# Performance work log

Hardware: AMD Instinct MI355X
Metric: run time of the kernel (lower is better)

Reference implementation:

```python
import jax, jax.numpy as jnp
import numpy as np

EMBED_DIM = 1024
HEAD_DIM = 64


def setup_inputs() -> dict:
    key = jax.random.key(0)
    k1, k2, k3, k4 = jax.random.split(key, 4)
    hidden_state = jax.random.normal(k1, (4, 4096, EMBED_DIM), dtype=jnp.float32)
    s = 1.0 / np.sqrt(EMBED_DIM)
    Wq = jax.random.uniform(k2, (EMBED_DIM, HEAD_DIM), dtype=jnp.float32, minval=-s, maxval=s)
    Wk = jax.random.uniform(k3, (EMBED_DIM, HEAD_DIM), dtype=jnp.float32, minval=-s, maxval=s)
    Wv = jax.random.uniform(k4, (EMBED_DIM, HEAD_DIM), dtype=jnp.float32, minval=-s, maxval=s)
    return {"hidden_state": hidden_state, "Wq": Wq, "Wk": Wk, "Wv": Wv}


def reference(hidden_state, Wq, Wk, Wv):
    # hidden_state: [B, S, E]; Wq/Wk/Wv: [E, D]
    q = hidden_state @ Wq  # [B, S, D]
    k = hidden_state @ Wk
    v = hidden_state @ Wv
    seq_len = hidden_state.shape[-2]
    scale = 1.0 / jnp.sqrt(jnp.asarray(HEAD_DIM, dtype=q.dtype))
    scores = jnp.einsum("bqd,bkd->bqk", q, k) * scale  # [B, S, S]
    causal = jnp.tril(jnp.ones((seq_len, seq_len), dtype=bool))  # [S, S]
    scores = jnp.where(causal[None, :, :], scores, jnp.asarray(-jnp.inf, dtype=scores.dtype))
    weights = jax.nn.softmax(scores, axis=-1)
    return jnp.einsum("bqk,bkd->bqd", weights, v)  # [B, S, D]
```

## Files before the change

kernel.cpp:

```cpp
#include <hip/hip_runtime.h>
#include <hip/hip_bf16.h>
#include <stdint.h>

#define SEQ 4096
#define EMB 1024
#define HD  64
#define NB  4

typedef __attribute__((ext_vector_type(8))) short short8;
typedef __attribute__((ext_vector_type(4))) float f32x4;
typedef __attribute__((ext_vector_type(4))) unsigned int uint4v;

static __device__ __forceinline__ unsigned short f2bf(float f) {
    unsigned int u = __float_as_uint(f);
    u += 0x7fffu + ((u >> 16) & 1u);
    return (unsigned short)(u >> 16);
}

__global__ __launch_bounds__(256) void wprep_kernel(
        const float* __restrict__ Wq, const float* __restrict__ Wk,
        const float* __restrict__ Wv, unsigned short* __restrict__ Wt) {
    int idx = blockIdx.x * 256 + threadIdx.x;
    int m = idx >> 16;
    int r = idx & 65535;
    int d = r >> 10;
    int e = r & 1023;
    const float* W = (m == 0) ? Wq : (m == 1) ? Wk : Wv;
    float v = W[e * HD + d];
    if (m == 0) v *= 0.18033688011111793f;
    Wt[idx] = f2bf(v);
}

__global__ __launch_bounds__(512, 4) void qkv_kernel(
        const float* __restrict__ H, const unsigned short* __restrict__ Wt,
        unsigned short* __restrict__ Qb, unsigned short* __restrict__ Kb,
        unsigned short* __restrict__ Vt) {
    __shared__ unsigned char smem[122880];
    unsigned short* ldsW = (unsigned short*)smem;
    float* ldsH = (float*)(smem + 3 * 24576);
    float* ldsO = (float*)smem;

    const int tid  = threadIdx.x;
    const int w    = tid >> 6;
    const int lane = tid & 63;
    const int lr = lane & 15, lg = lane >> 4;
    const int rt = w >> 1, ch = w & 1;
    const int rowbase = blockIdx.x * 64;

    f32x4 acc[6];
    #pragma unroll
    for (int nt = 0; nt < 6; ++nt) acc[nt] = f32x4{0.f, 0.f, 0.f, 0.f};

    auto stage = [&](int buf, int c) {
        const int kk0 = c * 64;
        #pragma unroll
        for (int ii = 0; ii < 3; ++ii) {
            int i = w * 3 + ii;
            int rowidx = 8 * i + (lane >> 3);
            int sb = (lane & 7) ^ (lane >> 3);
            const unsigned short* src = Wt + rowidx * EMB + kk0 + sb * 8;
            __builtin_amdgcn_global_load_lds(
                (const __attribute__((address_space(1))) void*)src,
                (__attribute__((address_space(3))) void*)(ldsW + buf * 12288 + i * 512 + lane * 8),
                16, 0, 0);
        }
        #pragma unroll
        for (int ii = 0; ii < 2; ++ii) {
            int i = w * 2 + ii;
            int rowidx = 4 * i + (lane >> 4);
            int key = rowidx & 7;
            int sb = (lane & 15) ^ key;
            const float* src = H + (size_t)(rowbase + rowidx) * EMB + kk0 + sb * 4;
            __builtin_amdgcn_global_load_lds(
                (const __attribute__((address_space(1))) void*)src,
                (__attribute__((address_space(3))) void*)(ldsH + buf * 4096 + i * 256 + lane * 4),
                16, 0, 0);
        }
    };

    auto compute = [&](int buf) {
        const int hrow = rt * 16 + lr;
        const int hkey = lr & 7;
        #pragma unroll
        for (int ks = 0; ks < 2; ++ks) {
            int b0 = ks * 8 + lg * 2;
            f32x4 h0 = *(const f32x4*)(ldsH + buf * 4096 + hrow * 64 + ((b0 ^ hkey) * 4));
            f32x4 h1 = *(const f32x4*)(ldsH + buf * 4096 + hrow * 64 + (((b0 + 1) ^ hkey) * 4));
            uint4v ua;
            asm("v_cvt_pk_bf16_f32 %0, %1, %2" : "=v"(ua[0]) : "v"(h0[0]), "v"(h0[1]));
            asm("v_cvt_pk_bf16_f32 %0, %1, %2" : "=v"(ua[1]) : "v"(h0[2]), "v"(h0[3]));
            asm("v_cvt_pk_bf16_f32 %0, %1, %2" : "=v"(ua[2]) : "v"(h1[0]), "v"(h1[1]));
            asm("v_cvt_pk_bf16_f32 %0, %1, %2" : "=v"(ua[3]) : "v"(h1[2]), "v"(h1[3]));
            short8 af = *(short8*)&ua;
            #pragma unroll
            for (int nt = 0; nt < 6; ++nt) {
                int f = ch * 6 + nt;
                int row = f * 16 + lr;
                int blk = (ks * 4 + lg) ^ hkey;
                short8 bf_ = *(const short8*)(ldsW + buf * 12288 + row * 64 + blk * 8);
                acc[nt] = __builtin_amdgcn_mfma_f32_16x16x32_bf16(af, bf_, acc[nt], 0, 0, 0);
            }
        }
    };

    stage(0, 0);
    stage(1, 1);
    for (int c = 0; c < 16; ++c) {
        if (c + 2 < 16) stage((c + 2) % 3, c + 2);
        if (c <= 13)      asm volatile("s_waitcnt vmcnt(10)" ::: "memory");
        else if (c == 14) asm volatile("s_waitcnt vmcnt(5)"  ::: "memory");
        else              asm volatile("s_waitcnt vmcnt(0)"  ::: "memory");
        __builtin_amdgcn_sched_barrier(0);
        __builtin_amdgcn_s_barrier();
        compute(c % 3);
        __builtin_amdgcn_s_barrier();
    }

    #pragma unroll
    for (int nt = 0; nt < 6; ++nt)
        #pragma unroll
        for (int r = 0; r < 4; ++r)
            ldsO[(rt * 16 + lg * 4 + r) * 200 + ch * 96 + nt * 16 + lr] = acc[nt][r];
    __syncthreads();

    {
        const int row = tid >> 3;
        const int d0  = (tid & 7) * 8;
        const size_t grow = (size_t)(rowbase + row);
        short8 uq, uk;
        #pragma unroll
        for (int j = 0; j < 8; ++j) {
            uq[j] = (short)f2bf(ldsO[row * 200 + d0 + j]);
            uk[j] = (short)f2bf(ldsO[row * 200 + 64 + d0 + j]);
        }
        *(short8*)(Qb + grow * HD + d0) = uq;
        *(short8*)(Kb + grow * HD + (d0 ^ ((row & 7) << 3))) = uk;
    }
    {
        const int d  = tid >> 3;
        const int j  = tid & 7;
        const int b  = rowbase >> 12;
        const int ci = (rowbase & (SEQ - 1)) >> 6;
        unsigned short* vrow = Vt + (((size_t)b * 64 + ci) * 64 + d) * 64;
        const int dsw = (d & 7) << 3;
        #pragma unroll
        for (int k4 = 0; k4 < 4; ++k4) {
            int t0 = j * 2 + k4 * 16;
            int tt = t0 & 31;
            int p0 = ((tt & 12) << 1) | (tt & 3) | ((tt & 16) >> 2);
            int e  = ((t0 & 32) | p0) ^ dsw;
            unsigned int val = (unsigned int)f2bf(ldsO[t0 * 200 + 128 + d])
                             | ((unsigned int)f2bf(ldsO[(t0 + 1) * 200 + 128 + d]) << 16);
            *(unsigned int*)(vrow + e) = val;
        }
    }
}

__global__ __launch_bounds__(512, 2) void attn_kernel(
        const unsigned short* __restrict__ Qb, const unsigned short* __restrict__ Kb,
        const unsigned short* __restrict__ Vt,
        float* __restrict__ part_o, float* __restrict__ part_l) {
    __shared__ unsigned short ldsK[3 * 64 * 64];
    __shared__ unsigned short ldsV[3 * 64 * 64];
    const int tid  = threadIdx.x;
    const int w    = tid >> 6;
    const int lane = tid & 63;
    const int lr = lane & 15, lg = lane >> 4;

    const int bid   = blockIdx.x;
    const int b     = bid & 3;
    const int qbr   = (bid >> 2) & 31;
    const int slice = bid >> 7;
    const int qb    = (slice >= 2) ? (31 - qbr) : qbr;
    const int qrow0 = qb * 128 + w * 16;
    const int qwmax = qrow0 + 15;

    const unsigned short* __restrict__ Kp = Kb + (size_t)b * SEQ * HD;
    const unsigned short* __restrict__ Vp = Vt + (size_t)b * 64 * 4096;
    const unsigned short* __restrict__ Qp = Qb + ((size_t)b * SEQ + qrow0) * HD;

    short8 qf0 = *(const short8*)(Qp + lr * HD +      lg * 8);
    short8 qf1 = *(const short8*)(Qp + lr * HD + 32 + lg * 8);

    f32x4 o[4];
    #pragma unroll
    for (int nt = 0; nt < 4; ++nt) o[nt] = f32x4{0.f, 0.f, 0.f, 0.f};
    float lrun = 0.f;

    const int T  = 2 * (qb + 1);
    const int sz = (T + 3) >> 2;
    const int c0 = slice * sz;
    const int c1 = (c0 + sz < T) ? (c0 + sz) : T;
    const int nch = c1 - c0;
    const int swz = (lr & 7) << 3;

    auto stage = [&](int buf, int it) {
        const unsigned short* gk = Kp + (size_t)it * 64 * HD + w * 512 + lane * 8;
        const unsigned short* gv = Vp + (size_t)it * 4096 + w * 512 + lane * 8;
        __builtin_amdgcn_global_load_lds(
            (const __attribute__((address_space(1))) void*)gk,
            (__attribute__((address_space(3))) void*)(ldsK + buf * 4096 + w * 512), 16, 0, 0);
        __builtin_amdgcn_global_load_lds(
            (const __attribute__((address_space(1))) void*)gv,
            (__attribute__((address_space(3))) void*)(ldsV + buf * 4096 + w * 512), 16, 0, 0);
    };

    if (nch > 0) {
        stage(0, c0);
        if (nch > 1) stage(1, c0 + 1);
        for (int i = 0; i < nch; ++i) {
            if (i + 2 < nch) stage((i + 2) % 3, c0 + i + 2);
            if (i + 2 < nch)      asm volatile("s_waitcnt vmcnt(4)" ::: "memory");
            else if (i + 1 < nch) asm volatile("s_waitcnt vmcnt(2)" ::: "memory");
            else                  asm volatile("s_waitcnt vmcnt(0)" ::: "memory");
            __builtin_amdgcn_sched_barrier(0);
            __builtin_amdgcn_s_barrier();

            const int kvb = (c0 + i) * 64;
            const int bufo = (i % 3) * 4096;
            if (kvb <= qwmax) {
                f32x4 s0 = f32x4{0.f, 0.f, 0.f, 0.f};
                f32x4 s1 = f32x4{0.f, 0.f, 0.f, 0.f};
                f32x4 s2 = f32x4{0.f, 0.f, 0.f, 0.f};
                f32x4 s3 = f32x4{0.f, 0.f, 0.f, 0.f};
                {
                    short8 ka0 = *(const short8*)&ldsK[bufo + (0 * 16 + lr) * 64 + ((lg * 8)      ^ swz)];
                    short8 kb0 = *(const short8*)&ldsK[bufo + (0 * 16 + lr) * 64 + ((lg * 8 + 32) ^ swz)];
                    short8 ka1 = *(const short8*)&ldsK[bufo + (1 * 16 + lr) * 64 + ((lg * 8)      ^ swz)];
                    short8 kb1 = *(const short8*)&ldsK[bufo + (1 * 16 + lr) * 64 + ((lg * 8 + 32) ^ swz)];
                    short8 ka2 = *(const short8*)&ldsK[bufo + (2 * 16 + lr) * 64 + ((lg * 8)      ^ swz)];
                    short8 kb2 = *(const short8*)&ldsK[bufo + (2 * 16 + lr) * 64 + ((lg * 8 + 32) ^ swz)];
                    short8 ka3 = *(const short8*)&ldsK[bufo + (3 * 16 + lr) * 64 + ((lg * 8)      ^ swz)];
                    short8 kb3 = *(const short8*)&ldsK[bufo + (3 * 16 + lr) * 64 + ((lg * 8 + 32) ^ swz)];
                    s0 = __builtin_amdgcn_mfma_f32_16x16x32_bf16(ka0, qf0, s0, 0, 0, 0);
                    s0 = __builtin_amdgcn_mfma_f32_16x16x32_bf16(kb0, qf1, s0, 0, 0, 0);
                    s1 = __builtin_amdgcn_mfma_f32_16x16x32_bf16(ka1, qf0, s1, 0, 0, 0);
                    s1 = __builtin_amdgcn_mfma_f32_16x16x32_bf16(kb1, qf1, s1, 0, 0, 0);
                    s2 = __builtin_amdgcn_mfma_f32_16x16x32_bf16(ka2, qf0, s2, 0, 0, 0);
                    s2 = __builtin_amdgcn_mfma_f32_16x16x32_bf16(kb2, qf1, s2, 0, 0, 0);
                    s3 = __builtin_amdgcn_mfma_f32_16x16x32_bf16(ka3, qf0, s3, 0, 0, 0);
                    s3 = __builtin_amdgcn_mfma_f32_16x16x32_bf16(kb3, qf1, s3, 0, 0, 0);
                }

                if (kvb + 63 > qrow0) {
                    const int qg = qrow0 + lr;
                    #pragma unroll
                    for (int r = 0; r < 4; ++r) {
                        int ky = kvb + lg * 4 + r;
                        if (ky      > qg) s0[r] = -1e30f;
                        if (ky + 16 > qg) s1[r] = -1e30f;
                        if (ky + 32 > qg) s2[r] = -1e30f;
                        if (ky + 48 > qg) s3[r] = -1e30f;
                    }
                }

                float p0[4], p1[4], p2[4], p3[4];
                #pragma unroll
                for (int r = 0; r < 4; ++r) {
                    p0[r] = exp2f(s0[r]);
                    p1[r] = exp2f(s1[r]);
                    p2[r] = exp2f(s2[r]);
                    p3[r] = exp2f(s3[r]);
                }
                lrun += ((p0[0] + p0[1]) + (p0[2] + p0[3])) + ((p1[0] + p1[1]) + (p1[2] + p1[3]))
                      + ((p2[0] + p2[1]) + (p2[2] + p2[3])) + ((p3[0] + p3[1]) + (p3[2] + p3[3]));

                uint4v ua, ub;
                asm("v_cvt_pk_bf16_f32 %0, %1, %2" : "=v"(ua[0]) : "v"(p0[0]), "v"(p0[1]));
                asm("v_cvt_pk_bf16_f32 %0, %1, %2" : "=v"(ua[1]) : "v"(p0[2]), "v"(p0[3]));
                asm("v_cvt_pk_bf16_f32 %0, %1, %2" : "=v"(ua[2]) : "v"(p1[0]), "v"(p1[1]));
                asm("v_cvt_pk_bf16_f32 %0, %1, %2" : "=v"(ua[3]) : "v"(p1[2]), "v"(p1[3]));
                asm("v_cvt_pk_bf16_f32 %0, %1, %2" : "=v"(ub[0]) : "v"(p2[0]), "v"(p2[1]));
                asm("v_cvt_pk_bf16_f32 %0, %1, %2" : "=v"(ub[1]) : "v"(p2[2]), "v"(p2[3]));
                asm("v_cvt_pk_bf16_f32 %0, %1, %2" : "=v"(ub[2]) : "v"(p3[0]), "v"(p3[1]));
                asm("v_cvt_pk_bf16_f32 %0, %1, %2" : "=v"(ub[3]) : "v"(p3[2]), "v"(p3[3]));
                short8 pba = *(short8*)&ua;
                short8 pbb = *(short8*)&ub;

                short8 va0 = *(const short8*)&ldsV[bufo + (0 * 16 + lr) * 64 + ((lg * 8)      ^ swz)];
                short8 vb0 = *(const short8*)&ldsV[bufo + (0 * 16 + lr) * 64 + ((lg * 8 + 32) ^ swz)];
                short8 va1 = *(const short8*)&ldsV[bufo + (1 * 16 + lr) * 64 + ((lg * 8)      ^ swz)];
                short8 vb1 = *(const short8*)&ldsV[bufo + (1 * 16 + lr) * 64 + ((lg * 8 + 32) ^ swz)];
                short8 va2 = *(const short8*)&ldsV[bufo + (2 * 16 + lr) * 64 + ((lg * 8)      ^ swz)];
                short8 vb2 = *(const short8*)&ldsV[bufo + (2 * 16 + lr) * 64 + ((lg * 8 + 32) ^ swz)];
                short8 va3 = *(const short8*)&ldsV[bufo + (3 * 16 + lr) * 64 + ((lg * 8)      ^ swz)];
                short8 vb3 = *(const short8*)&ldsV[bufo + (3 * 16 + lr) * 64 + ((lg * 8 + 32) ^ swz)];
                o[0] = __builtin_amdgcn_mfma_f32_16x16x32_bf16(va0, pba, o[0], 0, 0, 0);
                o[1] = __builtin_amdgcn_mfma_f32_16x16x32_bf16(va1, pba, o[1], 0, 0, 0);
                o[2] = __builtin_amdgcn_mfma_f32_16x16x32_bf16(va2, pba, o[2], 0, 0, 0);
                o[3] = __builtin_amdgcn_mfma_f32_16x16x32_bf16(va3, pba, o[3], 0, 0, 0);
                o[0] = __builtin_amdgcn_mfma_f32_16x16x32_bf16(vb0, pbb, o[0], 0, 0, 0);
                o[1] = __builtin_amdgcn_mfma_f32_16x16x32_bf16(vb1, pbb, o[1], 0, 0, 0);
                o[2] = __builtin_amdgcn_mfma_f32_16x16x32_bf16(vb2, pbb, o[2], 0, 0, 0);
                o[3] = __builtin_amdgcn_mfma_f32_16x16x32_bf16(vb3, pbb, o[3], 0, 0, 0);
            }
            __builtin_amdgcn_s_barrier();
        }
    }

    lrun += __shfl_xor(lrun, 16);
    lrun += __shfl_xor(lrun, 32);

    const size_t prow = (((size_t)slice * 4 + b) * 32 + qb) * 128 + w * 16 + lr;
    float* po = part_o + prow * 64;
    #pragma unroll
    for (int nt = 0; nt < 4; ++nt)
        *(f32x4*)(po + nt * 16 + lg * 4) = o[nt];
    if (lg == 0) part_l[prow] = lrun;
}

__global__ __launch_bounds__(256) void merge_kernel(
        const float* __restrict__ part_o, const float* __restrict__ part_l,
        float* __restrict__ out) {
    int idx = blockIdx.x * 256 + threadIdx.x;
    int d4  = (idx & 15) * 4;
    int row = idx >> 4;
    f32x4 a = f32x4{0.f, 0.f, 0.f, 0.f};
    float L = 0.f;
    #pragma unroll
    for (int s = 0; s < 4; ++s) {
        f32x4 p = *(const f32x4*)(part_o + ((size_t)s * 16384 + row) * 64 + d4);
        a[0] += p[0]; a[1] += p[1]; a[2] += p[2]; a[3] += p[3];
        L += part_l[s * 16384 + row];
    }
    float inv = 1.0f / L;
    f32x4 r;
    r[0] = a[0] * inv;
    r[1] = a[1] * inv;
    r[2] = a[2] * inv;
    r[3] = a[3] * inv;
    *(f32x4*)(out + (size_t)row * 64 + d4) = r;
}

extern "C" void kernel_launch(void* const* d_in, const int* in_sizes, int n_in,
                              void* d_out, int out_size, void* d_ws, size_t ws_size,
                              hipStream_t stream) {
    const float* H  = (const float*)d_in[0];
    const float* Wq = (const float*)d_in[1];
    const float* Wk = (const float*)d_in[2];
    const float* Wv = (const float*)d_in[3];
    float* out = (float*)d_out;

    unsigned short* Qb = (unsigned short*)d_ws;
    unsigned short* Kb = Qb + (size_t)NB * SEQ * HD;
    unsigned short* Vt = Kb + (size_t)NB * SEQ * HD;
    unsigned short* Wt = Vt + (size_t)NB * SEQ * HD;
    float* part_o = (float*)(Wt + 3 * 65536);
    float* part_l = part_o + (size_t)4 * 16384 * 64;

    wprep_kernel<<<768, 256, 0, stream>>>(Wq, Wk, Wv, Wt);
    qkv_kernel<<<NB * SEQ / 64, 512, 0, stream>>>(H, Wt, Qb, Kb, Vt);
    attn_kernel<<<512, 512, 0, stream>>>(Qb, Kb, Vt, part_o, part_l);
    merge_kernel<<<1024, 256, 0, stream>>>(part_o, part_l, out);
}
```

Baseline: 52.65 us.

## Stage KV tiles in pairs with double buffering to halve barriers

Restructures the attention loop so each iteration loads and processes two 64-row K/V tiles. A two-slot double buffer replaces the three-slot single-tile ring, which halves the number of workgroup barriers and waitcnt points per chunk. LDS per block grows from 48KB to 64KB, which may reduce occupancy at two blocks per CU. The prefetch distance in tiles stays similar, but each wait now covers a larger batch.

```diff
diff --git a/kernel.cpp b/kernel.cpp
--- a/kernel.cpp
+++ b/kernel.cpp
@@ -160,8 +160,8 @@
         const unsigned short* __restrict__ Qb, const unsigned short* __restrict__ Kb,
         const unsigned short* __restrict__ Vt,
         float* __restrict__ part_o, float* __restrict__ part_l) {
-    __shared__ unsigned short ldsK[3 * 64 * 64];
-    __shared__ unsigned short ldsV[3 * 64 * 64];
+    __shared__ unsigned short ldsK[2 * 2 * 4096];
+    __shared__ unsigned short ldsV[2 * 2 * 4096];
     const int tid  = threadIdx.x;
     const int w    = tid >> 6;
     const int lane = tid & 63;
@@ -192,107 +192,123 @@
     const int c0 = slice * sz;
     const int c1 = (c0 + sz < T) ? (c0 + sz) : T;
     const int nch = c1 - c0;
+    const int nin = (nch + 1) >> 1;
+    const bool tail_odd = (nch & 1) != 0;
     const int swz = (lr & 7) << 3;
 
-    auto stage = [&](int buf, int it) {
-        const unsigned short* gk = Kp + (size_t)it * 64 * HD + w * 512 + lane * 8;
-        const unsigned short* gv = Vp + (size_t)it * 4096 + w * 512 + lane * 8;
-        __builtin_amdgcn_global_load_lds(
-            (const __attribute__((address_space(1))) void*)gk,
-            (__attribute__((address_space(3))) void*)(ldsK + buf * 4096 + w * 512), 16, 0, 0);
-        __builtin_amdgcn_global_load_lds(
-            (const __attribute__((address_space(1))) void*)gv,
-            (__attribute__((address_space(3))) void*)(ldsV + buf * 4096 + w * 512), 16, 0, 0);
+    auto stage_pair = [&](int buf, int j) {
+        #pragma unroll
+        for (int jj = 0; jj < 2; ++jj) {
+            int ci = c0 + 2 * j + jj;
+            if (ci < c1) {
+                const unsigned short* gk = Kp + (size_t)ci * 64 * HD + w * 512 + lane * 8;
+                const unsigned short* gv = Vp + (size_t)ci * 4096 + w * 512 + lane * 8;
+                __builtin_amdgcn_global_load_lds(
+                    (const __attribute__((address_space(1))) void*)gk,
+                    (__attribute__((address_space(3))) void*)(ldsK + buf * 8192 + jj * 4096 + w * 512), 16, 0, 0);
+                __builtin_amdgcn_global_load_lds(
+                    (const __attribute__((address_space(1))) void*)gv,
+                    (__attribute__((address_space(3))) void*)(ldsV + buf * 8192 + jj * 4096 + w * 512), 16, 0, 0);
+            }
+        }
     };
 
     if (nch > 0) {
-        stage(0, c0);
-        if (nch > 1) stage(1, c0 + 1);
-        for (int i = 0; i < nch; ++i) {
-            if (i + 2 < nch) stage((i + 2) % 3, c0 + i + 2);
-            if (i + 2 < nch)      asm volatile("s_waitcnt vmcnt(4)" ::: "memory");
-            else if (i + 1 < nch) asm volatile("s_waitcnt vmcnt(2)" ::: "memory");
-            else                  asm volatile("s_waitcnt vmcnt(0)" ::: "memory");
+        stage_pair(0, 0);
+        for (int j = 0; j < nin; ++j) {
+            if (j + 1 < nin) stage_pair((j + 1) & 1, j + 1);
+            if (j + 1 < nin) {
+                if (tail_odd && (j + 2 == nin)) asm volatile("s_waitcnt vmcnt(2)" ::: "memory");
+                else                            asm volatile("s_waitcnt vmcnt(4)" ::: "memory");
+            } else {
+                asm volatile("s_waitcnt vmcnt(0)" ::: "memory");
+            }
             __builtin_amdgcn_sched_barrier(0);
             __builtin_amdgcn_s_barrier();
 
-            const int kvb = (c0 + i) * 64;
-            const int bufo = (i % 3) * 4096;
-            if (kvb <= qwmax) {
-                f32x4 s0 = f32x4{0.f, 0.f, 0.f, 0.f};
-                f32x4 s1 = f32x4{0.f, 0.f, 0.f, 0.f};
-                f32x4 s2 = f32x4{0.f, 0.f, 0.f, 0.f};
-                f32x4 s3 = f32x4{0.f, 0.f, 0.f, 0.f};
-                {
-                    short8 ka0 = *(const short8*)&ldsK[bufo + (0 * 16 + lr) * 64 + ((lg * 8)      ^ swz)];
-                    short8 kb0 = *(const short8*)&ldsK[bufo + (0 * 16 + lr) * 64 + ((lg * 8 + 32) ^ swz)];
-                    short8 ka1 = *(const short8*)&ldsK[bufo + (1 * 16 + lr) * 64 + ((lg * 8)      ^ swz)];
-                    short8 kb1 = *(const short8*)&ldsK[bufo + (1 * 16 + lr) * 64 + ((lg * 8 + 32) ^ swz)];
-                    short8 ka2 = *(const short8*)&ldsK[bufo + (2 * 16 + lr) * 64 + ((lg * 8)      ^ swz)];
-                    short8 kb2 = *(const short8*)&ldsK[bufo + (2 * 16 + lr) * 64 + ((lg * 8 + 32) ^ swz)];
-                    short8 ka3 = *(const short8*)&ldsK[bufo + (3 * 16 + lr) * 64 + ((lg * 8)      ^ swz)];
-                    short8 kb3 = *(const short8*)&ldsK[bufo + (3 * 16 + lr) * 64 + ((lg * 8 + 32) ^ swz)];
-                    s0 = __builtin_amdgcn_mfma_f32_16x16x32_bf16(ka0, qf0, s0, 0, 0, 0);
-                    s0 = __builtin_amdgcn_mfma_f32_16x16x32_bf16(kb0, qf1, s0, 0, 0, 0);
-                    s1 = __builtin_amdgcn_mfma_f32_16x16x32_bf16(ka1, qf0, s1, 0, 0, 0);
-                    s1 = __builtin_amdgcn_mfma_f32_16x16x32_bf16(kb1, qf1, s1, 0, 0, 0);
-                    s2 = __builtin_amdgcn_mfma_f32_16x16x32_bf16(ka2, qf0, s2, 0, 0, 0);
-                    s2 = __builtin_amdgcn_mfma_f32_16x16x32_bf16(kb2, qf1, s2, 0, 0, 0);
-                    s3 = __builtin_amdgcn_mfma_f32_16x16x32_bf16(ka3, qf0, s3, 0, 0, 0);
-                    s3 = __builtin_amdgcn_mfma_f32_16x16x32_bf16(kb3, qf1, s3, 0, 0, 0);
-                }
-
-                if (kvb + 63 > qrow0) {
-                    const int qg = qrow0 + lr;
-                    #pragma unroll
-                    for (int r = 0; r < 4; ++r) {
-                        int ky = kvb + lg * 4 + r;
-                        if (ky      > qg) s0[r] = -1e30f;
-                        if (ky + 16 > qg) s1[r] = -1e30f;
-                        if (ky + 32 > qg) s2[r] = -1e30f;
-                        if (ky + 48 > qg) s3[r] = -1e30f;
+            #pragma unroll
+            for (int jj = 0; jj < 2; ++jj) {
+                const int ci = c0 + 2 * j + jj;
+                if (ci < c1) {
+                    const int kvb = ci * 64;
+                    const int bufo = ((j & 1) * 2 + jj) * 4096;
+                    if (kvb <= qwmax) {
+                        f32x4 s0 = f32x4{0.f, 0.f, 0.f, 0.f};
+                        f32x4 s1 = f32x4{0.f, 0.f, 0.f, 0.f};
+                        f32x4 s2 = f32x4{0.f, 0.f, 0.f, 0.f};
+                        f32x4 s3 = f32x4{0.f, 0.f, 0.f, 0.f};
+                        {
+                            short8 ka0 = *(const short8*)&ldsK[bufo + (0 * 16 + lr) * 64 + ((lg * 8)      ^ swz)];
+                            short8 kb0 = *(const short8*)&ldsK[bufo + (0 * 16 + lr) * 64 + ((lg * 8 + 32) ^ swz)];
+                            short8 ka1 = *(const short8*)&ldsK[bufo + (1 * 16 + lr) * 64 + ((lg * 8)      ^ swz)];
+                            short8 kb1 = *(const short8*)&ldsK[bufo + (1 * 16 + lr) * 64 + ((lg * 8 + 32) ^ swz)];
+                            short8 ka2 = *(const short8*)&ldsK[bufo + (2 * 16 + lr) * 64 + ((lg * 8)      ^ swz)];
+                            short8 kb2 = *(const short8*)&ldsK[bufo + (2 * 16 + lr) * 64 + ((lg * 8 + 32) ^ swz)];
+                            short8 ka3 = *(const short8*)&ldsK[bufo + (3 * 16 + lr) * 64 + ((lg * 8)      ^ swz)];
+                            short8 kb3 = *(const short8*)&ldsK[bufo + (3 * 16 + lr) * 64 + ((lg * 8 + 32) ^ swz)];
+                            s0 = __builtin_amdgcn_mfma_f32_16x16x32_bf16(ka0, qf0, s0, 0, 0, 0);
+                            s0 = __builtin_amdgcn_mfma_f32_16x16x32_bf16(kb0, qf1, s0, 0, 0, 0);
+                            s1 = __builtin_amdgcn_mfma_f32_16x16x32_bf16(ka1, qf0, s1, 0, 0, 0);
+                            s1 = __builtin_amdgcn_mfma_f32_16x16x32_bf16(kb1, qf1, s1, 0, 0, 0);
+                            s2 = __builtin_amdgcn_mfma_f32_16x16x32_bf16(ka2, qf0, s2, 0, 0, 0);
+                            s2 = __builtin_amdgcn_mfma_f32_16x16x32_bf16(kb2, qf1, s2, 0, 0, 0);
+                            s3 = __builtin_amdgcn_mfma_f32_16x16x32_bf16(ka3, qf0, s3, 0, 0, 0);
+                            s3 = __builtin_amdgcn_mfma_f32_16x16x32_bf16(kb3, qf1, s3, 0, 0, 0);
+                        }
+
+                        if (kvb + 63 > qrow0) {
+                            const int qg = qrow0 + lr;
+                            #pragma unroll
+                            for (int r = 0; r < 4; ++r) {
+                                int ky = kvb + lg * 4 + r;
+                                if (ky      > qg) s0[r] = -1e30f;
+                                if (ky + 16 > qg) s1[r] = -1e30f;
+                                if (ky + 32 > qg) s2[r] = -1e30f;
+                                if (ky + 48 > qg) s3[r] = -1e30f;
+                            }
+                        }
+
+                        float p0[4], p1[4], p2[4], p3[4];
+                        #pragma unroll
+                        for (int r = 0; r < 4; ++r) {
+                            p0[r] = exp2f(s0[r]);
+                            p1[r] = exp2f(s1[r]);
+                            p2[r] = exp2f(s2[r]);
+                            p3[r] = exp2f(s3[r]);
+                        }
+                        lrun += ((p0[0] + p0[1]) + (p0[2] + p0[3])) + ((p1[0] + p1[1]) + (p1[2] + p1[3]))
+                              + ((p2[0] + p2[1]) + (p2[2] + p2[3])) + ((p3[0] + p3[1]) + (p3[2] + p3[3]));
+
+                        uint4v ua, ub;
+                        asm("v_cvt_pk_bf16_f32 %0, %1, %2" : "=v"(ua[0]) : "v"(p0[0]), "v"(p0[1]));
+                        asm("v_cvt_pk_bf16_f32 %0, %1, %2" : "=v"(ua[1]) : "v"(p0[2]), "v"(p0[3]));
+                        asm("v_cvt_pk_bf16_f32 %0, %1, %2" : "=v"(ua[2]) : "v"(p1[0]), "v"(p1[1]));
+                        asm("v_cvt_pk_bf16_f32 %0, %1, %2" : "=v"(ua[3]) : "v"(p1[2]), "v"(p1[3]));
+                        asm("v_cvt_pk_bf16_f32 %0, %1, %2" : "=v"(ub[0]) : "v"(p2[0]), "v"(p2[1]));
+                        asm("v_cvt_pk_bf16_f32 %0, %1, %2" : "=v"(ub[1]) : "v"(p2[2]), "v"(p2[3]));
+                        asm("v_cvt_pk_bf16_f32 %0, %1, %2" : "=v"(ub[2]) : "v"(p3[0]), "v"(p3[1]));
+                        asm("v_cvt_pk_bf16_f32 %0, %1, %2" : "=v"(ub[3]) : "v"(p3[2]), "v"(p3[3]));
+                        short8 pba = *(short8*)&ua;
+                        short8 pbb = *(short8*)&ub;
+
+                        short8 va0 = *(const short8*)&ldsV[bufo + (0 * 16 + lr) * 64 + ((lg * 8)      ^ swz)];
+                        short8 vb0 = *(const short8*)&ldsV[bufo + (0 * 16 + lr) * 64 + ((lg * 8 + 32) ^ swz)];
+                        short8 va1 = *(const short8*)&ldsV[bufo + (1 * 16 + lr) * 64 + ((lg * 8)      ^ swz)];
+                        short8 vb1 = *(const short8*)&ldsV[bufo + (1 * 16 + lr) * 64 + ((lg * 8 + 32) ^ swz)];
+                        short8 va2 = *(const short8*)&ldsV[bufo + (2 * 16 + lr) * 64 + ((lg * 8)      ^ swz)];
+                        short8 vb2 = *(const short8*)&ldsV[bufo + (2 * 16 + lr) * 64 + ((lg * 8 + 32) ^ swz)];
+                        short8 va3 = *(const short8*)&ldsV[bufo + (3 * 16 + lr) * 64 + ((lg * 8)      ^ swz)];
+                        short8 vb3 = *(const short8*)&ldsV[bufo + (3 * 16 + lr) * 64 + ((lg * 8 + 32) ^ swz)];
+                        o[0] = __builtin_amdgcn_mfma_f32_16x16x32_bf16(va0, pba, o[0], 0, 0, 0);
+                        o[1] = __builtin_amdgcn_mfma_f32_16x16x32_bf16(va1, pba, o[1], 0, 0, 0);
+                        o[2] = __builtin_amdgcn_mfma_f32_16x16x32_bf16(va2, pba, o[2], 0, 0, 0);
+                        o[3] = __builtin_amdgcn_mfma_f32_16x16x32_bf16(va3, pba, o[3], 0, 0, 0);
+                        o[0] = __builtin_amdgcn_mfma_f32_16x16x32_bf16(vb0, pbb, o[0], 0, 0, 0);
+                        o[1] = __builtin_amdgcn_mfma_f32_16x16x32_bf16(vb1, pbb, o[1], 0, 0, 0);
+                        o[2] = __builtin_amdgcn_mfma_f32_16x16x32_bf16(vb2, pbb, o[2], 0, 0, 0);
+                        o[3] = __builtin_amdgcn_mfma_f32_16x16x32_bf16(vb3, pbb, o[3], 0, 0, 0);
                     }
                 }
-
-                float p0[4], p1[4], p2[4], p3[4];
-                #pragma unroll
-                for (int r = 0; r < 4; ++r) {
-                    p0[r] = exp2f(s0[r]);
-                    p1[r] = exp2f(s1[r]);
-                    p2[r] = exp2f(s2[r]);
-                    p3[r] = exp2f(s3[r]);
-                }
-                lrun += ((p0[0] + p0[1]) + (p0[2] + p0[3])) + ((p1[0] + p1[1]) + (p1[2] + p1[3]))
-                      + ((p2[0] + p2[1]) + (p2[2] + p2[3])) + ((p3[0] + p3[1]) + (p3[2] + p3[3]));
-
-                uint4v ua, ub;
-                asm("v_cvt_pk_bf16_f32 %0, %1, %2" : "=v"(ua[0]) : "v"(p0[0]), "v"(p0[1]));
-                asm("v_cvt_pk_bf16_f32 %0, %1, %2" : "=v"(ua[1]) : "v"(p0[2]), "v"(p0[3]));
-                asm("v_cvt_pk_bf16_f32 %0, %1, %2" : "=v"(ua[2]) : "v"(p1[0]), "v"(p1[1]));
-                asm("v_cvt_pk_bf16_f32 %0, %1, %2" : "=v"(ua[3]) : "v"(p1[2]), "v"(p1[3]));
-                asm("v_cvt_pk_bf16_f32 %0, %1, %2" : "=v"(ub[0]) : "v"(p2[0]), "v"(p2[1]));
-                asm("v_cvt_pk_bf16_f32 %0, %1, %2" : "=v"(ub[1]) : "v"(p2[2]), "v"(p2[3]));
-                asm("v_cvt_pk_bf16_f32 %0, %1, %2" : "=v"(ub[2]) : "v"(p3[0]), "v"(p3[1]));
-                asm("v_cvt_pk_bf16_f32 %0, %1, %2" : "=v"(ub[3]) : "v"(p3[2]), "v"(p3[3]));
-                short8 pba = *(short8*)&ua;
-                short8 pbb = *(short8*)&ub;
-
-                short8 va0 = *(const short8*)&ldsV[bufo + (0 * 16 + lr) * 64 + ((lg * 8)      ^ swz)];
-                short8 vb0 = *(const short8*)&ldsV[bufo + (0 * 16 + lr) * 64 + ((lg * 8 + 32) ^ swz)];
-                short8 va1 = *(const short8*)&ldsV[bufo + (1 * 16 + lr) * 64 + ((lg * 8)      ^ swz)];
-                short8 vb1 = *(const short8*)&ldsV[bufo + (1 * 16 + lr) * 64 + ((lg * 8 + 32) ^ swz)];
-                short8 va2 = *(const short8*)&ldsV[bufo + (2 * 16 + lr) * 64 + ((lg * 8)      ^ swz)];
-                short8 vb2 = *(const short8*)&ldsV[bufo + (2 * 16 + lr) * 64 + ((lg * 8 + 32) ^ swz)];
-                short8 va3 = *(const short8*)&ldsV[bufo + (3 * 16 + lr) * 64 + ((lg * 8)      ^ swz)];
-                short8 vb3 = *(const short8*)&ldsV[bufo + (3 * 16 + lr) * 64 + ((lg * 8 + 32) ^ swz)];
-                o[0] = __builtin_amdgcn_mfma_f32_16x16x32_bf16(va0, pba, o[0], 0, 0, 0);
-                o[1] = __builtin_amdgcn_mfma_f32_16x16x32_bf16(va1, pba, o[1], 0, 0, 0);
-                o[2] = __builtin_amdgcn_mfma_f32_16x16x32_bf16(va2, pba, o[2], 0, 0, 0);
-                o[3] = __builtin_amdgcn_mfma_f32_16x16x32_bf16(va3, pba, o[3], 0, 0, 0);
-                o[0] = __builtin_amdgcn_mfma_f32_16x16x32_bf16(vb0, pbb, o[0], 0, 0, 0);
-                o[1] = __builtin_amdgcn_mfma_f32_16x16x32_bf16(vb1, pbb, o[1], 0, 0, 0);
-                o[2] = __builtin_amdgcn_mfma_f32_16x16x32_bf16(vb2, pbb, o[2], 0, 0, 0);
-                o[3] = __builtin_amdgcn_mfma_f32_16x16x32_bf16(vb3, pbb, o[3], 0, 0, 0);
             }
             __builtin_amdgcn_s_barrier();
         }
```

Measured after the change: 50.34 us (median of 2 runs). 4.4% less time.

## Process two query tiles per workgroup and split KV into eight slices

Applied to the files above, without the earlier changes.

Each attention workgroup now handles two 128-row query tiles that share each staged K/V chunk, so every LDS load of K and V feeds twice as many MFMAs. The KV range is split into eight slices instead of four, which keeps the grid at 512 blocks, and the launch-bounds occupancy hint rises from 2 to 4 blocks per CU. The merge kernel sums eight partials and the partial buffers double in size. The costs are higher register pressure from holding two Q fragments and two accumulator sets, and extra partial-result traffic in the merge.

```diff
diff --git a/kernel.cpp b/kernel.cpp
--- a/kernel.cpp
+++ b/kernel.cpp
@@ -156,12 +156,12 @@
     }
 }
 
-__global__ __launch_bounds__(512, 2) void attn_kernel(
+__global__ __launch_bounds__(512, 4) void attn_kernel(
         const unsigned short* __restrict__ Qb, const unsigned short* __restrict__ Kb,
         const unsigned short* __restrict__ Vt,
         float* __restrict__ part_o, float* __restrict__ part_l) {
-    __shared__ unsigned short ldsK[3 * 64 * 64];
-    __shared__ unsigned short ldsV[3 * 64 * 64];
+    __shared__ unsigned short ldsK[3 * 4096];
+    __shared__ unsigned short ldsV[3 * 4096];
     const int tid  = threadIdx.x;
     const int w    = tid >> 6;
     const int lane = tid & 63;
@@ -169,28 +169,31 @@
 
     const int bid   = blockIdx.x;
     const int b     = bid & 3;
-    const int qbr   = (bid >> 2) & 31;
-    const int slice = bid >> 7;
-    const int qb    = (slice >= 2) ? (31 - qbr) : qbr;
-    const int qrow0 = qb * 128 + w * 16;
-    const int qwmax = qrow0 + 15;
+    const int pr    = (bid >> 2) & 15;
+    const int slice = bid >> 6;
+    const int p     = (slice >= 4) ? (15 - pr) : pr;
+    const int qbase = p * 256;
+    const int qa0   = qbase + w * 16;
+    const int qb0   = qbase + 128 + w * 16;
 
     const unsigned short* __restrict__ Kp = Kb + (size_t)b * SEQ * HD;
     const unsigned short* __restrict__ Vp = Vt + (size_t)b * 64 * 4096;
-    const unsigned short* __restrict__ Qp = Qb + ((size_t)b * SEQ + qrow0) * HD;
-
-    short8 qf0 = *(const short8*)(Qp + lr * HD +      lg * 8);
-    short8 qf1 = *(const short8*)(Qp + lr * HD + 32 + lg * 8);
-
-    f32x4 o[4];
+    const unsigned short* __restrict__ Qp = Qb + (size_t)b * SEQ * HD;
+
+    short8 qfa0 = *(const short8*)(Qp + (size_t)(qa0 + lr) * HD +      lg * 8);
+    short8 qfa1 = *(const short8*)(Qp + (size_t)(qa0 + lr) * HD + 32 + lg * 8);
+    short8 qfb0 = *(const short8*)(Qp + (size_t)(qb0 + lr) * HD +      lg * 8);
+    short8 qfb1 = *(const short8*)(Qp + (size_t)(qb0 + lr) * HD + 32 + lg * 8);
+
+    f32x4 oA[4], oB[4];
     #pragma unroll
-    for (int nt = 0; nt < 4; ++nt) o[nt] = f32x4{0.f, 0.f, 0.f, 0.f};
-    float lrun = 0.f;
-
-    const int T  = 2 * (qb + 1);
-    const int sz = (T + 3) >> 2;
-    const int c0 = slice * sz;
-    const int c1 = (c0 + sz < T) ? (c0 + sz) : T;
+    for (int nt = 0; nt < 4; ++nt) { oA[nt] = f32x4{0.f,0.f,0.f,0.f}; oB[nt] = f32x4{0.f,0.f,0.f,0.f}; }
+    float lrunA = 0.f, lrunB = 0.f;
+
+    const int T   = 4 * (p + 1);
+    const int sz  = (T + 7) >> 3;
+    const int c0  = slice * sz;
+    const int c1  = (c0 + sz < T) ? (c0 + sz) : T;
     const int nch = c1 - c0;
     const int swz = (lr & 7) << 3;
 
@@ -218,32 +221,33 @@
 
             const int kvb = (c0 + i) * 64;
             const int bufo = (i % 3) * 4096;
-            if (kvb <= qwmax) {
-                f32x4 s0 = f32x4{0.f, 0.f, 0.f, 0.f};
-                f32x4 s1 = f32x4{0.f, 0.f, 0.f, 0.f};
-                f32x4 s2 = f32x4{0.f, 0.f, 0.f, 0.f};
-                f32x4 s3 = f32x4{0.f, 0.f, 0.f, 0.f};
-                {
-                    short8 ka0 = *(const short8*)&ldsK[bufo + (0 * 16 + lr) * 64 + ((lg * 8)      ^ swz)];
-                    short8 kb0 = *(const short8*)&ldsK[bufo + (0 * 16 + lr) * 64 + ((lg * 8 + 32) ^ swz)];
-                    short8 ka1 = *(const short8*)&ldsK[bufo + (1 * 16 + lr) * 64 + ((lg * 8)      ^ swz)];
-                    short8 kb1 = *(const short8*)&ldsK[bufo + (1 * 16 + lr) * 64 + ((lg * 8 + 32) ^ swz)];
-                    short8 ka2 = *(const short8*)&ldsK[bufo + (2 * 16 + lr) * 64 + ((lg * 8)      ^ swz)];
-                    short8 kb2 = *(const short8*)&ldsK[bufo + (2 * 16 + lr) * 64 + ((lg * 8 + 32) ^ swz)];
-                    short8 ka3 = *(const short8*)&ldsK[bufo + (3 * 16 + lr) * 64 + ((lg * 8)      ^ swz)];
-                    short8 kb3 = *(const short8*)&ldsK[bufo + (3 * 16 + lr) * 64 + ((lg * 8 + 32) ^ swz)];
-                    s0 = __builtin_amdgcn_mfma_f32_16x16x32_bf16(ka0, qf0, s0, 0, 0, 0);
-                    s0 = __builtin_amdgcn_mfma_f32_16x16x32_bf16(kb0, qf1, s0, 0, 0, 0);
-                    s1 = __builtin_amdgcn_mfma_f32_16x16x32_bf16(ka1, qf0, s1, 0, 0, 0);
-                    s1 = __builtin_amdgcn_mfma_f32_16x16x32_bf16(kb1, qf1, s1, 0, 0, 0);
-                    s2 = __builtin_amdgcn_mfma_f32_16x16x32_bf16(ka2, qf0, s2, 0, 0, 0);
-                    s2 = __builtin_amdgcn_mfma_f32_16x16x32_bf16(kb2, qf1, s2, 0, 0, 0);
-                    s3 = __builtin_amdgcn_mfma_f32_16x16x32_bf16(ka3, qf0, s3, 0, 0, 0);
-                    s3 = __builtin_amdgcn_mfma_f32_16x16x32_bf16(kb3, qf1, s3, 0, 0, 0);
-                }
-
-                if (kvb + 63 > qrow0) {
-                    const int qg = qrow0 + lr;
+
+            short8 ka0 = *(const short8*)&ldsK[bufo + (0 * 16 + lr) * 64 + ((lg * 8)      ^ swz)];
+            short8 kb0 = *(const short8*)&ldsK[bufo + (0 * 16 + lr) * 64 + ((lg * 8 + 32) ^ swz)];
+            short8 ka1 = *(const short8*)&ldsK[bufo + (1 * 16 + lr) * 64 + ((lg * 8)      ^ swz)];
+            short8 kb1 = *(const short8*)&ldsK[bufo + (1 * 16 + lr) * 64 + ((lg * 8 + 32) ^ swz)];
+            short8 ka2 = *(const short8*)&ldsK[bufo + (2 * 16 + lr) * 64 + ((lg * 8)      ^ swz)];
+            short8 kb2 = *(const short8*)&ldsK[bufo + (2 * 16 + lr) * 64 + ((lg * 8 + 32) ^ swz)];
+            short8 ka3 = *(const short8*)&ldsK[bufo + (3 * 16 + lr) * 64 + ((lg * 8)      ^ swz)];
+            short8 kb3 = *(const short8*)&ldsK[bufo + (3 * 16 + lr) * 64 + ((lg * 8 + 32) ^ swz)];
+
+            short8 pbaA, pbbA, pbaB, pbbB;
+            bool doA = (kvb <= qa0 + 15);
+            bool doB = (kvb <= qb0 + 15);
+
+            if (doA) {
+                f32x4 s0 = f32x4{0.f,0.f,0.f,0.f}, s1 = f32x4{0.f,0.f,0.f,0.f};
+                f32x4 s2 = f32x4{0.f,0.f,0.f,0.f}, s3 = f32x4{0.f,0.f,0.f,0.f};
+                s0 = __builtin_amdgcn_mfma_f32_16x16x32_bf16(ka0, qfa0, s0, 0, 0, 0);
+                s0 = __builtin_amdgcn_mfma_f32_16x16x32_bf16(kb0, qfa1, s0, 0, 0, 0);
+                s1 = __builtin_amdgcn_mfma_f32_16x16x32_bf16(ka1, qfa0, s1, 0, 0, 0);
+                s1 = __builtin_amdgcn_mfma_f32_16x16x32_bf16(kb1, qfa1, s1, 0, 0, 0);
+                s2 = __builtin_amdgcn_mfma_f32_16x16x32_bf16(ka2, qfa0, s2, 0, 0, 0);
+                s2 = __builtin_amdgcn_mfma_f32_16x16x32_bf16(kb2, qfa1, s2, 0, 0, 0);
+                s3 = __builtin_amdgcn_mfma_f32_16x16x32_bf16(ka3, qfa0, s3, 0, 0, 0);
+                s3 = __builtin_amdgcn_mfma_f32_16x16x32_bf16(kb3, qfa1, s3, 0, 0, 0);
+                if (kvb + 63 > qa0) {
+                    const int qg = qa0 + lr;
                     #pragma unroll
                     for (int r = 0; r < 4; ++r) {
                         int ky = kvb + lg * 4 + r;
@@ -253,18 +257,14 @@
                         if (ky + 48 > qg) s3[r] = -1e30f;
                     }
                 }
-
                 float p0[4], p1[4], p2[4], p3[4];
                 #pragma unroll
                 for (int r = 0; r < 4; ++r) {
-                    p0[r] = exp2f(s0[r]);
-                    p1[r] = exp2f(s1[r]);
-                    p2[r] = exp2f(s2[r]);
-                    p3[r] = exp2f(s3[r]);
-                }
-                lrun += ((p0[0] + p0[1]) + (p0[2] + p0[3])) + ((p1[0] + p1[1]) + (p1[2] + p1[3]))
-                      + ((p2[0] + p2[1]) + (p2[2] + p2[3])) + ((p3[0] + p3[1]) + (p3[2] + p3[3]));
-
+                    p0[r] = exp2f(s0[r]); p1[r] = exp2f(s1[r]);
+                    p2[r] = exp2f(s2[r]); p3[r] = exp2f(s3[r]);
+                }
+                lrunA += ((p0[0]+p0[1])+(p0[2]+p0[3])) + ((p1[0]+p1[1])+(p1[2]+p1[3]))
+                       + ((p2[0]+p2[1])+(p2[2]+p2[3])) + ((p3[0]+p3[1])+(p3[2]+p3[3]));
                 uint4v ua, ub;
                 asm("v_cvt_pk_bf16_f32 %0, %1, %2" : "=v"(ua[0]) : "v"(p0[0]), "v"(p0[1]));
                 asm("v_cvt_pk_bf16_f32 %0, %1, %2" : "=v"(ua[1]) : "v"(p0[2]), "v"(p0[3]));
@@ -274,39 +274,111 @@
                 asm("v_cvt_pk_bf16_f32 %0, %1, %2" : "=v"(ub[1]) : "v"(p2[2]), "v"(p2[3]));
                 asm("v_cvt_pk_bf16_f32 %0, %1, %2" : "=v"(ub[2]) : "v"(p3[0]), "v"(p3[1]));
                 asm("v_cvt_pk_bf16_f32 %0, %1, %2" : "=v"(ub[3]) : "v"(p3[2]), "v"(p3[3]));
-                short8 pba = *(short8*)&ua;
-                short8 pbb = *(short8*)&ub;
-
-                short8 va0 = *(const short8*)&ldsV[bufo + (0 * 16 + lr) * 64 + ((lg * 8)      ^ swz)];
+                pbaA = *(short8*)&ua;  pbbA = *(short8*)&ub;
+            }
+            if (doB) {
+                f32x4 s0 = f32x4{0.f,0.f,0.f,0.f}, s1 = f32x4{0.f,0.f,0.f,0.f};
+                f32x4 s2 = f32x4{0.f,0.f,0.f,0.f}, s3 = f32x4{0.f,0.f,0.f,0.f};
+                s0 = __builtin_amdgcn_mfma_f32_16x16x32_bf16(ka0, qfb0, s0, 0, 0, 0);
+                s0 = __builtin_amdgcn_mfma_f32_16x16x32_bf16(kb0, qfb1, s0, 0, 0, 0);
+                s1 = __builtin_amdgcn_mfma_f32_16x16x32_bf16(ka1, qfb0, s1, 0, 0, 0);
+                s1 = __builtin_amdgcn_mfma_f32_16x16x32_bf16(kb1, qfb1, s1, 0, 0, 0);
+                s2 = __builtin_amdgcn_mfma_f32_16x16x32_bf16(ka2, qfb0, s2, 0, 0, 0);
+                s2 = __builtin_amdgcn_mfma_f32_16x16x32_bf16(kb2, qfb1, s2, 0, 0, 0);
+                s3 = __builtin_amdgcn_mfma_f32_16x16x32_bf16(ka3, qfb0, s3, 0, 0, 0);
+                s3 = __builtin_amdgcn_mfma_f32_16x16x32_bf16(kb3, qfb1, s3, 0, 0, 0);
+                if (kvb + 63 > qb0) {
+                    const int qg = qb0 + lr;
+                    #pragma unroll
+                    for (int r = 0; r < 4; ++r) {
+                        int ky = kvb + lg * 4 + r;
+                        if (ky      > qg) s0[r] = -1e30f;
+                        if (ky + 16 > qg) s1[r] = -1e30f;
+                        if (ky + 32 > qg) s2[r] = -1e30f;
+                        if (ky + 48 > qg) s3[r] = -1e30f;
+                    }
+                }
+                float p0[4], p1[4], p2[4], p3[4];
+                #pragma unroll
+                for (int r = 0; r < 4; ++r) {
+                    p0[r] = exp2f(s0[r]); p1[r] = exp2f(s1[r]);
+                    p2[r] = exp2f(s2[r]); p3[r] = exp2f(s3[r]);
+                }
+                lrunB += ((p0[0]+p0[1])+(p0[2]+p0[3])) + ((p1[0]+p1[1])+(p1[2]+p1[3]))
+                       + ((p2[0]+p2[1])+(p2[2]+p2[3])) + ((p3[0]+p3[1])+(p3[2]+p3[3]));
+                uint4v ua, ub;
+                asm("v_cvt_pk_bf16_f32 %0, %1, %2" : "=v"(ua[0]) : "v"(p0[0]), "v"(p0[1]));
+                asm("v_cvt_pk_bf16_f32 %0, %1, %2" : "=v"(ua[1]) : "v"(p0[2]), "v"(p0[3]));
+                asm("v_cvt_pk_bf16_f32 %0, %1, %2" : "=v"(ua[2]) : "v"(p1[0]), "v"(p1[1]));
+                asm("v_cvt_pk_bf16_f32 %0, %1, %2" : "=v"(ua[3]) : "v"(p1[2]), "v"(p1[3]));
+                asm("v_cvt_pk_bf16_f32 %0, %1, %2" : "=v"(ub[0]) : "v"(p2[0]), "v"(p2[1]));
+                asm("v_cvt_pk_bf16_f32 %0, %1, %2" : "=v"(ub[1]) : "v"(p2[2]), "v"(p2[3]));
+                asm("v_cvt_pk_bf16_f32 %0, %1, %2" : "=v"(ub[2]) : "v"(p3[0]), "v"(p3[1]));
+                asm("v_cvt_pk_bf16_f32 %0, %1, %2" : "=v"(ub[3]) : "v"(p3[2]), "v"(p3[3]));
+                pbaB = *(short8*)&ua;  pbbB = *(short8*)&ub;
+            }
+
+            {
+                short8 va0 = *(const short8*)&ldsV[bufo + (0 * 16 + lr) * 64 + ((lg * 8) ^ swz)];
+                short8 va1 = *(const short8*)&ldsV[bufo + (1 * 16 + lr) * 64 + ((lg * 8) ^ swz)];
+                short8 va2 = *(const short8*)&ldsV[bufo + (2 * 16 + lr) * 64 + ((lg * 8) ^ swz)];
+                short8 va3 = *(const short8*)&ldsV[bufo + (3 * 16 + lr) * 64 + ((lg * 8) ^ swz)];
+                if (doA) {
+                    oA[0] = __builtin_amdgcn_mfma_f32_16x16x32_bf16(va0, pbaA, oA[0], 0, 0, 0);
+                    oA[1] = __builtin_amdgcn_mfma_f32_16x16x32_bf16(va1, pbaA, oA[1], 0, 0, 0);
+                    oA[2] = __builtin_amdgcn_mfma_f32_16x16x32_bf16(va2, pbaA, oA[2], 0, 0, 0);
+                    oA[3] = __builtin_amdgcn_mfma_f32_16x16x32_bf16(va3, pbaA, oA[3], 0, 0, 0);
+                }
+                if (doB) {
+                    oB[0] = __builtin_amdgcn_mfma_f32_16x16x32_bf16(va0, pbaB, oB[0], 0, 0, 0);
+                    oB[1] = __builtin_amdgcn_mfma_f32_16x16x32_bf16(va1, pbaB, oB[1], 0, 0, 0);
+                    oB[2] = __builtin_amdgcn_mfma_f32_16x16x32_bf16(va2, pbaB, oB[2], 0, 0, 0);
+                    oB[3] = __builtin_amdgcn_mfma_f32_16x16x32_bf16(va3, pbaB, oB[3], 0, 0, 0);
+                }
+            }
+            {
                 short8 vb0 = *(const short8*)&ldsV[bufo + (0 * 16 + lr) * 64 + ((lg * 8 + 32) ^ swz)];
-                short8 va1 = *(const short8*)&ldsV[bufo + (1 * 16 + lr) * 64 + ((lg * 8)      ^ swz)];
                 short8 vb1 = *(const short8*)&ldsV[bufo + (1 * 16 + lr) * 64 + ((lg * 8 + 32) ^ swz)];
-                short8 va2 = *(const short8*)&ldsV[bufo + (2 * 16 + lr) * 64 + ((lg * 8)      ^ swz)];
                 short8 vb2 = *(const short8*)&ldsV[bufo + (2 * 16 + lr) * 64 + ((lg * 8 + 32) ^ swz)];
-                short8 va3 = *(const short8*)&ldsV[bufo + (3 * 16 + lr) * 64 + ((lg * 8)      ^ swz)];
                 short8 vb3 = *(const short8*)&ldsV[bufo + (3 * 16 + lr) * 64 + ((lg * 8 + 32) ^ swz)];
-                o[0] = __builtin_amdgcn_mfma_f32_16x16x32_bf16(va0, pba, o[0], 0, 0, 0);
-                o[1] = __builtin_amdgcn_mfma_f32_16x16x32_bf16(va1, pba, o[1], 0, 0, 0);
-                o[2] = __builtin_amdgcn_mfma_f32_16x16x32_bf16(va2, pba, o[2], 0, 0, 0);
-                o[3] = __builtin_amdgcn_mfma_f32_16x16x32_bf16(va3, pba, o[3], 0, 0, 0);
-                o[0] = __builtin_amdgcn_mfma_f32_16x16x32_bf16(vb0, pbb, o[0], 0, 0, 0);
-                o[1] = __builtin_amdgcn_mfma_f32_16x16x32_bf16(vb1, pbb, o[1], 0, 0, 0);
-                o[2] = __builtin_amdgcn_mfma_f32_16x16x32_bf16(vb2, pbb, o[2], 0, 0, 0);
-                o[3] = __builtin_amdgcn_mfma_f32_16x16x32_bf16(vb3, pbb, o[3], 0, 0, 0);
+                if (doA) {
+                    oA[0] = __builtin_amdgcn_mfma_f32_16x16x32_bf16(vb0, pbbA, oA[0], 0, 0, 0);
+                    oA[1] = __builtin_amdgcn_mfma_f32_16x16x32_bf16(vb1, pbbA, oA[1], 0, 0, 0);
+                    oA[2] = __builtin_amdgcn_mfma_f32_16x16x32_bf16(vb2, pbbA, oA[2], 0, 0, 0);
+                    oA[3] = __builtin_amdgcn_mfma_f32_16x16x32_bf16(vb3, pbbA, oA[3], 0, 0, 0);
+                }
+                if (doB) {
+                    oB[0] = __builtin_amdgcn_mfma_f32_16x16x32_bf16(vb0, pbbB, oB[0], 0, 0, 0);
+                    oB[1] = __builtin_amdgcn_mfma_f32_16x16x32_bf16(vb1, pbbB, oB[1], 0, 0, 0);
+                    oB[2] = __builtin_amdgcn_mfma_f32_16x16x32_bf16(vb2, pbbB, oB[2], 0, 0, 0);
+                    oB[3] = __builtin_amdgcn_mfma_f32_16x16x32_bf16(vb3, pbbB, oB[3], 0, 0, 0);
+                }
             }
             __builtin_amdgcn_s_barrier();
         }
     }
 
-    lrun += __shfl_xor(lrun, 16);
-    lrun += __shfl_xor(lrun, 32);
-
-    const size_t prow = (((size_t)slice * 4 + b) * 32 + qb) * 128 + w * 16 + lr;
-    float* po = part_o + prow * 64;
-    #pragma unroll
-    for (int nt = 0; nt < 4; ++nt)
-        *(f32x4*)(po + nt * 16 + lg * 4) = o[nt];
-    if (lg == 0) part_l[prow] = lrun;
+    lrunA += __shfl_xor(lrunA, 16);
+    lrunA += __shfl_xor(lrunA, 32);
+    lrunB += __shfl_xor(lrunB, 16);
+    lrunB += __shfl_xor(lrunB, 32);
+
+    {
+        const size_t prowA = ((size_t)slice * 4 + b) * 4096 + qa0 + lr;
+        float* po = part_o + prowA * 64;
+        #pragma unroll
+        for (int nt = 0; nt < 4; ++nt)
+            *(f32x4*)(po + nt * 16 + lg * 4) = oA[nt];
+        if (lg == 0) part_l[prowA] = lrunA;
+    }
+    {
+        const size_t prowB = ((size_t)slice * 4 + b) * 4096 + qb0 + lr;
+        float* po = part_o + prowB * 64;
+        #pragma unroll
+        for (int nt = 0; nt < 4; ++nt)
+            *(f32x4*)(po + nt * 16 + lg * 4) = oB[nt];
+        if (lg == 0) part_l[prowB] = lrunB;
+    }
 }
 
 __global__ __launch_bounds__(256) void merge_kernel(
@@ -318,7 +390,7 @@
     f32x4 a = f32x4{0.f, 0.f, 0.f, 0.f};
     float L = 0.f;
     #pragma unroll
-    for (int s = 0; s < 4; ++s) {
+    for (int s = 0; s < 8; ++s) {
         f32x4 p = *(const f32x4*)(part_o + ((size_t)s * 16384 + row) * 64 + d4);
         a[0] += p[0]; a[1] += p[1]; a[2] += p[2]; a[3] += p[3];
         L += part_l[s * 16384 + row];
@@ -346,7 +418,7 @@
     unsigned short* Vt = Kb + (size_t)NB * SEQ * HD;
     unsigned short* Wt = Vt + (size_t)NB * SEQ * HD;
     float* part_o = (float*)(Wt + 3 * 65536);
-    float* part_l = part_o + (size_t)4 * 16384 * 64;
+    float* part_l = part_o + (size_t)8 * 16384 * 64;
 
     wprep_kernel<<<768, 256, 0, stream>>>(Wq, Wk, Wv, Wt);
     qkv_kernel<<<NB * SEQ / 64, 512, 0, stream>>>(H, Wt, Qb, Kb, Vt);
```

New measurement: 56.08 us. 6.5% more time.
